# Kernel optimization log

Measured on AMD Instinct MI355X. Metric: run time of the kernel, lower is better.

Reference implementation:

```python
import jax, jax.numpy as jnp
import numpy as np
from jax import lax

B, L, NCH, NQ, NL, FW, NCLS = 256, 3000, 4, 8, 2, 128, 5
BN_EPS = 1e-5


def setup_inputs() -> dict:
    key = jax.random.key(0)
    ks = jax.random.split(key, 24)
    rn = lambda k, shape, s=0.05: jax.random.normal(k, shape, jnp.float32) * s
    inp = {}
    inp['x'] = jax.random.normal(ks[0], (B, NCH, L), jnp.float32)
    inp['conv1_w'] = rn(ks[1], (32, NCH, 7)); inp['conv1_b'] = rn(ks[2], (32,))
    inp['bn1_g'] = 1.0 + rn(ks[3], (32,)); inp['bn1_b'] = rn(ks[3], (32,))
    inp['conv2_w'] = rn(ks[4], (64, 32, 7)); inp['conv2_b'] = rn(ks[5], (64,))
    inp['bn2_g'] = 1.0 + rn(ks[6], (64,)); inp['bn2_b'] = rn(ks[6], (64,))
    inp['conv3_w'] = rn(ks[7], (128, 64, 7)); inp['conv3_b'] = rn(ks[8], (128,))
    inp['bn3_g'] = 1.0 + rn(ks[9], (128,)); inp['bn3_b'] = rn(ks[9], (128,))
    inp['conv4_w'] = rn(ks[10], (128, 128, 7)); inp['conv4_b'] = rn(ks[11], (128,))
    inp['bn4_g'] = 1.0 + rn(ks[12], (128,)); inp['bn4_b'] = rn(ks[12], (128,))
    inp['fc_w'] = rn(ks[13], (FW, 128)); inp['fc_b'] = rn(ks[14], (FW,))
    inp['ang_w'] = rn(ks[15], (NQ, FW)); inp['ang_b'] = rn(ks[16], (NQ,))
    # TorchLayer default init: uniform in [0, 2*pi)
    inp['qw'] = jax.random.uniform(ks[17], (NL, NQ, 3), jnp.float32, 0.0, 2.0 * np.pi)
    inp['h1_w'] = rn(ks[18], (64, NQ)); inp['h1_b'] = rn(ks[19], (64,))
    inp['h2_w'] = rn(ks[20], (NCLS, 64)); inp['h2_b'] = rn(ks[21], (NCLS,))
    return inp


def _conv1d(x, w, b):
    y = lax.conv_general_dilated(x, w, (1,), [(3, 3)], dimension_numbers=('NCH', 'OIH', 'NCH'))
    return y + b[None, :, None]


def _bn(x, g, b):  # eval-mode BN: running_mean=0, running_var=1
    inv = 1.0 / np.sqrt(1.0 + BN_EPS)
    return x * (g * inv)[None, :, None] + b[None, :, None]


def _maxpool4(x):
    return lax.reduce_window(x, -jnp.inf, lax.max, (1, 1, 4), (1, 1, 4), 'VALID')


def _apply_1q(state, U, w, batched):
    # state: (B, 2**NQ); wire 0 = most significant bit (PennyLane convention)
    bs = state.shape[0]
    st = state.reshape(bs, 2 ** w, 2, -1)
    if batched:
        new = jnp.einsum('sab,slbr->slar', U, st)
    else:
        new = jnp.einsum('ab,slbr->slar', U, st)
    return new.reshape(bs, -1)


def _apply_cnot(state, c, t):
    bs = state.shape[0]
    q1, q2 = min(c, t), max(c, t)
    s = state.reshape(bs, 2 ** q1, 2, 2 ** (q2 - q1 - 1), 2, -1)
    ci, ti = (2, 4) if c < t else (4, 2)
    c0 = lax.index_in_dim(s, 0, ci, keepdims=True)
    c1 = jnp.flip(lax.index_in_dim(s, 1, ci, keepdims=True), axis=ti)
    return jnp.concatenate([c0, c1], axis=ci).reshape(bs, -1)


def _rot_matrix(phi, th, om):
    # PennyLane Rot(phi, theta, omega) = RZ(omega) RY(theta) RZ(phi)
    cm, sm = jnp.cos(th / 2), jnp.sin(th / 2)
    m00 = jnp.exp(-0.5j * (phi + om)) * cm
    m01 = -jnp.exp(0.5j * (phi - om)) * sm
    m10 = jnp.exp(-0.5j * (phi - om)) * sm
    m11 = jnp.exp(0.5j * (phi + om)) * cm
    return jnp.stack([jnp.stack([m00, m01]), jnp.stack([m10, m11])]).astype(jnp.complex64)


def _qsim(angles, qw):
    bs = angles.shape[0]
    dim = 2 ** NQ
    state = jnp.zeros((bs, dim), jnp.complex64).at[:, 0].set(1.0)
    # AngleEmbedding: RY(angle_w) on each wire (batched matrices)
    c, s = jnp.cos(angles / 2), jnp.sin(angles / 2)
    for w in range(NQ):
        U = jnp.stack([jnp.stack([c[:, w], -s[:, w]], -1),
                       jnp.stack([s[:, w], c[:, w]], -1)], -2).astype(jnp.complex64)
        state = _apply_1q(state, U, w, batched=True)
    # StronglyEntanglingLayers: Rot on each wire, then CNOT ring with range r
    for l in range(NL):
        for w in range(NQ):
            U = _rot_matrix(qw[l, w, 0], qw[l, w, 1], qw[l, w, 2])
            state = _apply_1q(state, U, w, batched=False)
        r = (l % (NQ - 1)) + 1
        for i in range(NQ):
            state = _apply_cnot(state, i, (i + r) % NQ)
    probs = state.real ** 2 + state.imag ** 2
    z = [probs.reshape(bs, 2 ** w, 2, -1)[:, :, 0].sum((1, 2))
         - probs.reshape(bs, 2 ** w, 2, -1)[:, :, 1].sum((1, 2)) for w in range(NQ)]
    return jnp.stack(z, -1)  # (B, NQ)


def reference(x, conv1_w, conv1_b, bn1_g, bn1_b, conv2_w, conv2_b, bn2_g, bn2_b,
              conv3_w, conv3_b, bn3_g, bn3_b, conv4_w, conv4_b, bn4_g, bn4_b,
              fc_w, fc_b, ang_w, ang_b, qw, h1_w, h1_b, h2_w, h2_b):
    h = jax.nn.relu(_bn(_conv1d(x, conv1_w, conv1_b), bn1_g, bn1_b))
    h = jax.nn.relu(_bn(_conv1d(h, conv2_w, conv2_b), bn2_g, bn2_b))
    h = _maxpool4(h)
    h = jax.nn.relu(_bn(_conv1d(h, conv3_w, conv3_b), bn3_g, bn3_b))
    h = _maxpool4(h)
    h = jax.nn.relu(_bn(_conv1d(h, conv4_w, conv4_b), bn4_g, bn4_b))
    h = h.mean(-1)  # AdaptiveAvgPool1d(1) + Flatten -> (B, 128)
    h = jax.nn.relu(h @ fc_w.T + fc_b)  # Dropout is identity in eval
    raw = h @ ang_w.T + ang_b
    angles = np.pi * jnp.tanh(raw)
    q = _qsim(angles, qw)
    h2 = jax.nn.relu(q @ h1_w.T + h1_b)
    return h2 @ h2_w.T + h2_b
```

## Files before the change

kernel.cpp:

```cpp
#include <hip/hip_runtime.h>
#include <hip/hip_bf16.h>

#define BN_INV 0.9999950000375f
#define PI_F   3.14159265358979f

typedef __attribute__((ext_vector_type(8))) short s16x8;
typedef __attribute__((ext_vector_type(4))) float f32x4;
typedef __attribute__((ext_vector_type(4))) unsigned short u16x4;

__device__ inline unsigned short f2bf(float f) {
  union { float f; unsigned u; } v; v.f = f;
  unsigned r = v.u + 0x7fffu + ((v.u >> 16) & 1u);
  return (unsigned short)(r >> 16);
}

__global__ __launch_bounds__(256) void k_packumat(
    const float* __restrict__ w1, const float* __restrict__ w2,
    const float* __restrict__ w3, const float* __restrict__ w4,
    const float* __restrict__ fcw, const float* __restrict__ qw,
    unsigned short* __restrict__ w1p, unsigned short* __restrict__ w2p,
    unsigned short* __restrict__ w3p, unsigned short* __restrict__ w4p,
    float* __restrict__ fcwt, float* __restrict__ h4,
    float2* __restrict__ Ut)
{
  __shared__ float rotm[16][8];
  const int tid = threadIdx.x;

  if (blockIdx.x < 928) {
    int e = blockIdx.x * 256 + tid;
    if (e < 2048) {
      int co = e >> 6, k = e & 63, kk = k >> 3, ci = k & 7;
      w1p[e] = (ci < 4 && kk < 7) ? f2bf(w1[co * 28 + ci * 7 + kk]) : (unsigned short)0;
    } else if (e < 16384) {
      int t = e - 2048; int co = t / 224, k = t % 224, kk = k >> 5, ci = k & 31;
      w2p[t] = f2bf(w2[co * 224 + ci * 7 + kk]);
    } else if (e < 73728) {
      int t = e - 16384; int co = t / 448, k = t % 448, kk = k >> 6, ci = k & 63;
      w3p[t] = f2bf(w3[co * 448 + ci * 7 + kk]);
    } else if (e < 188416) {
      int t = e - 73728; int co = t / 896, k = t % 896, kk = k >> 7, ci = k & 127;
      w4p[t] = f2bf(w4[co * 896 + ci * 7 + kk]);
    } else if (e < 221184) {
      h4[e - 188416] = 0.f;
    } else if (e < 237568) {
      int t = e - 221184; int k = t >> 7, o = t & 127;
      fcwt[t] = fcw[o * 128 + k];
    }
    return;
  }

  const int bx = blockIdx.x - 928;
  if (tid < 16) {
    int gq = tid;
    float phi = qw[gq * 3], th = qw[gq * 3 + 1], om = qw[gq * 3 + 2];
    float cm = cosf(0.5f * th), sm = sinf(0.5f * th);
    float ap = 0.5f * (phi + om), bm = 0.5f * (phi - om);
    rotm[gq][0] = cm * cosf(ap);  rotm[gq][1] = -cm * sinf(ap);
    rotm[gq][2] = -sm * cosf(bm); rotm[gq][3] = -sm * sinf(bm);
    rotm[gq][4] = sm * cosf(bm);  rotm[gq][5] = -sm * sinf(bm);
    rotm[gq][6] = cm * cosf(ap);  rotm[gq][7] = cm * sinf(ap);
  }
  __syncthreads();

  const int lane = tid & 63, wid = tid >> 6;
  const int ll = lane & 15;
  const int c = (bx * 4 + wid) * 4 + (lane >> 4);

  float2 st[16];
  #pragma unroll
  for (int r = 0; r < 16; ++r) {
    st[r].x = (ll == (c >> 4) && r == (c & 15)) ? 1.f : 0.f;
    st[r].y = 0.f;
  }

#define LOADM(G) \
  float m00x = rotm[G][0], m00y = rotm[G][1], m01x = rotm[G][2], m01y = rotm[G][3], \
        m10x = rotm[G][4], m10y = rotm[G][5], m11x = rotm[G][6], m11y = rotm[G][7];

#define ROT_REG(G, BETA) { LOADM(G) \
  _Pragma("unroll") \
  for (int r = 0; r < 16; ++r) if (!(r & BETA)) { \
    float2 A = st[r], B = st[r + BETA]; \
    st[r].x = m00x*A.x - m00y*A.y + m01x*B.x - m01y*B.y; \
    st[r].y = m00x*A.y + m00y*A.x + m01x*B.y + m01y*B.x; \
    st[r+BETA].x = m10x*A.x - m10y*A.y + m11x*B.x - m11y*B.y; \
    st[r+BETA].y = m10x*A.y + m10y*A.x + m11x*B.y + m11y*B.x; } }

#define ROT_LANE(G, LX) { LOADM(G) \
  _Pragma("unroll") \
  for (int r = 0; r < 16; ++r) { \
    float ox = __shfl_xor(st[r].x, LX); \
    float oy = __shfl_xor(st[r].y, LX); \
    bool hi = (lane & LX) != 0; \
    float a0x = hi ? ox : st[r].x, a0y = hi ? oy : st[r].y; \
    float a1x = hi ? st[r].x : ox, a1y = hi ? st[r].y : oy; \
    float cx = hi ? m10x : m00x, cy = hi ? m10y : m00y; \
    float dx = hi ? m11x : m01x, dy = hi ? m11y : m01y; \
    st[r].x = cx*a0x - cy*a0y + dx*a1x - dy*a1y; \
    st[r].y = cx*a0y + cy*a0x + dx*a1y + dy*a1x; } }

#define CNOT_RR(BC, BT) { \
  _Pragma("unroll") \
  for (int r = 0; r < 16; ++r) if ((r & BC) && !(r & BT)) { \
    float2 t_ = st[r]; st[r] = st[r + BT]; st[r + BT] = t_; } }

#define CNOT_RL(BC, LXT) { \
  _Pragma("unroll") \
  for (int r = 0; r < 16; ++r) if (r & BC) { \
    st[r].x = __shfl_xor(st[r].x, LXT); \
    st[r].y = __shfl_xor(st[r].y, LXT); } }

#define CNOT_LR(LXC, BT) { bool cc = (lane & LXC) != 0; \
  _Pragma("unroll") \
  for (int r = 0; r < 16; ++r) if (!(r & BT)) { \
    float2 A = st[r], B = st[r + BT]; \
    st[r].x = cc ? B.x : A.x;  st[r].y = cc ? B.y : A.y; \
    st[r+BT].x = cc ? A.x : B.x;  st[r+BT].y = cc ? A.y : B.y; } }

#define CNOT_LL(LXC, LXT) { bool cc = (lane & LXC) != 0; \
  _Pragma("unroll") \
  for (int r = 0; r < 16; ++r) { \
    float ox = __shfl_xor(st[r].x, LXT); \
    float oy = __shfl_xor(st[r].y, LXT); \
    if (cc) { st[r].x = ox; st[r].y = oy; } } }

  ROT_LANE(0, 8) ROT_LANE(1, 4) ROT_LANE(2, 2) ROT_LANE(3, 1)
  ROT_REG(4, 8)  ROT_REG(5, 4)  ROT_REG(6, 2)  ROT_REG(7, 1)
  CNOT_LL(8, 4) CNOT_LL(4, 2) CNOT_LL(2, 1) CNOT_LR(1, 8)
  CNOT_RR(8, 4) CNOT_RR(4, 2) CNOT_RR(2, 1) CNOT_RL(1, 8)
  ROT_LANE(8, 8) ROT_LANE(9, 4) ROT_LANE(10, 2) ROT_LANE(11, 1)
  ROT_REG(12, 8) ROT_REG(13, 4) ROT_REG(14, 2)  ROT_REG(15, 1)
  CNOT_LL(8, 2) CNOT_LL(4, 1) CNOT_LR(2, 8) CNOT_LR(1, 4)
  CNOT_RR(8, 2) CNOT_RR(4, 1) CNOT_RL(2, 8) CNOT_RL(1, 4)

#undef LOADM
#undef ROT_REG
#undef ROT_LANE
#undef CNOT_RR
#undef CNOT_RL
#undef CNOT_LR
#undef CNOT_LL

  float2* uc = Ut + c * 256 + ll * 16;
  #pragma unroll
  for (int r = 0; r < 16; r += 2) {
    float4 v = make_float4(st[r].x, st[r].y, st[r + 1].x, st[r + 1].y);
    *(float4*)(uc + r) = v;
  }
}

__global__ __launch_bounds__(512) void k_conv12(
    const float* __restrict__ x, const unsigned short* __restrict__ w1p,
    const unsigned short* __restrict__ w2p,
    const float* __restrict__ c1b, const float* __restrict__ b1g,
    const float* __restrict__ b1b,
    const float* __restrict__ c2b, const float* __restrict__ b2g,
    const float* __restrict__ b2b,
    unsigned short* __restrict__ h2pt)
{
  __shared__ __align__(16) char lds[71296];
  const int XR = 0;
  const int H1 = 8576;
  const int W2 = 41856;
  float* s1 = (float*)(lds + 70528);
  float* s2 = (float*)(lds + 70784);

  const int tid = threadIdx.x, b = blockIdx.y;
  const int l0 = blockIdx.x * 512;

  for (int r = tid; r < 536; r += 512) {
    int gp = l0 - 6 + r;
    s16x8 v;
    for (int i = 0; i < 8; ++i) v[i] = 0;
    if (r < 524 && gp >= 0 && gp < 3000) {
      const float* xr = x + b * 4 * 3000 + gp;
      v[0] = (short)f2bf(xr[0]);
      v[1] = (short)f2bf(xr[3000]);
      v[2] = (short)f2bf(xr[6000]);
      v[3] = (short)f2bf(xr[9000]);
    }
    *(s16x8*)(lds + XR + r * 16) = v;
  }
  for (int e = tid; e < 1792; e += 512) {
    int co = e / 28, cc = e % 28;
    s16x8 v = *(const s16x8*)(w2p + co * 224 + cc * 8);
    *(s16x8*)(lds + W2 + ((co * 448 + cc * 16) ^ ((co & 7) << 4))) = v;
  }
  if (tid < 32) {
    float sc = b1g[tid] * BN_INV;
    s1[tid * 2] = sc;
    s1[tid * 2 + 1] = fmaf(c1b[tid], sc, b1b[tid]);
  }
  if (tid < 64) {
    float sc = b2g[tid] * BN_INV;
    s2[tid * 2] = sc;
    s2[tid * 2 + 1] = fmaf(c2b[tid], sc, b2b[tid]);
  }
  __syncthreads();

  const int w = tid >> 6, lane = tid & 63, lr = lane & 15, g = lane >> 4;

  {
    s16x8 a1[2][2];
    #pragma unroll
    for (int m = 0; m < 2; ++m)
      #pragma unroll
      for (int s = 0; s < 2; ++s)
        a1[m][s] = *(const s16x8*)(w1p + (m * 16 + lr) * 64 + s * 32 + g * 8);

    #pragma unroll
    for (int t = 0; t < 5; ++t) {
      int tile = w + t * 8;
      if (tile >= 33) break;
      int p0 = tile * 16;
      f32x4 acc[2];
      for (int m = 0; m < 2; ++m)
        for (int i = 0; i < 4; ++i) acc[m][i] = 0.f;
      #pragma unroll
      for (int s = 0; s < 2; ++s) {
        s16x8 bf = *(const s16x8*)(lds + XR + (p0 + lr + s * 4 + g) * 16);
        acc[0] = __builtin_amdgcn_mfma_f32_16x16x32_bf16(a1[0][s], bf, acc[0], 0, 0, 0);
        acc[1] = __builtin_amdgcn_mfma_f32_16x16x32_bf16(a1[1][s], bf, acc[1], 0, 0, 0);
      }
      int r2 = p0 + lr;
      if (r2 < 518) {
        #pragma unroll
        for (int m = 0; m < 2; ++m) {
          int co0 = m * 16 + g * 4;
          u16x4 o;
          #pragma unroll
          for (int j = 0; j < 4; ++j)
            o[j] = f2bf(fmaxf(fmaf(acc[m][j], s1[(co0 + j) * 2], s1[(co0 + j) * 2 + 1]), 0.f));
          int byte = ((r2 * 64 + (co0 >> 3) * 16) ^ ((r2 & 7) << 4)) + (co0 & 7) * 2;
          *(u16x4*)(lds + H1 + byte) = o;
        }
      }
    }
  }
  __syncthreads();

  const int wp = w * 64;
  f32x4 acc[4][4];
  for (int m = 0; m < 4; ++m)
    for (int n = 0; n < 4; ++n)
      for (int i = 0; i < 4; ++i) acc[m][n][i] = 0.f;

  #pragma unroll
  for (int s = 0; s < 7; ++s) {
    s16x8 xa[4], wb[4];
    #pragma unroll
    for (int m = 0; m < 4; ++m) {
      int row = wp + m * 16 + lr + s;
      xa[m] = *(const s16x8*)(lds + H1 + ((row * 64 + g * 16) ^ ((row & 7) << 4)));
    }
    #pragma unroll
    for (int n = 0; n < 4; ++n) {
      int co = n * 16 + lr;
      wb[n] = *(const s16x8*)(lds + W2 + ((co * 448 + s * 64 + g * 16) ^ ((co & 7) << 4)));
    }
    #pragma unroll
    for (int m = 0; m < 4; ++m)
      #pragma unroll
      for (int n = 0; n < 4; ++n)
        acc[m][n] = __builtin_amdgcn_mfma_f32_16x16x32_bf16(xa[m], wb[n], acc[m][n], 0, 0, 0);
  }

  float sc[4], sh[4];
  #pragma unroll
  for (int n = 0; n < 4; ++n) {
    sc[n] = s2[(n * 16 + lr) * 2];
    sh[n] = s2[(n * 16 + lr) * 2 + 1];
  }
  #pragma unroll
  for (int m = 0; m < 4; ++m) {
    int pp = (l0 + wp + m * 16 + g * 4) >> 2;
    if (pp < 750) {
      unsigned short* orow = h2pt + (b * 750 + pp) * 64 + lr;
      #pragma unroll
      for (int n = 0; n < 4; ++n) {
        float v = fmaxf(fmaxf(acc[m][n][0], acc[m][n][1]),
                        fmaxf(acc[m][n][2], acc[m][n][3]));
        orow[n * 16] = f2bf(fmaxf(fmaf(v, sc[n], sh[n]), 0.f));
      }
    }
  }
}

__global__ __launch_bounds__(256) void k_conv3(
    const unsigned short* __restrict__ h2pt, const unsigned short* __restrict__ w3p,
    const float* __restrict__ cb, const float* __restrict__ bng,
    const float* __restrict__ bnb, unsigned short* __restrict__ h3pt)
{
  __shared__ __align__(16) char lds[75776];
  float* scs = (float*)(lds + 74752);
  const int tid = threadIdx.x, b = blockIdx.y;
  const int l0 = blockIdx.x * 128;

  for (int e = tid; e < 1072; e += 256) {
    int r = e >> 3, c = e & 7;
    int gr = l0 + r - 3;
    s16x8 v;
    if (gr >= 0 && gr < 750) v = *(const s16x8*)(h2pt + (b * 750 + gr) * 64 + c * 8);
    else for (int i = 0; i < 8; ++i) v[i] = 0;
    *(s16x8*)(lds + ((r * 128 + c * 16) ^ ((r & 7) << 4))) = v;
  }
  for (int e = tid; e < 3584; e += 256) {
    int co = e / 28, c = e % 28;
    s16x8 v = *(const s16x8*)(w3p + co * 448 + c * 8);
    *(s16x8*)(lds + 17408 + ((co * 448 + c * 16) ^ ((co & 7) << 4))) = v;
  }
  if (tid < 128) {
    float sc = bng[tid] * BN_INV;
    scs[tid * 2] = sc;
    scs[tid * 2 + 1] = fmaf(cb[tid], sc, bnb[tid]);
  }

  const int lane = tid & 63, wid = tid >> 6;
  const int wr = wid >> 1, wc = wid & 1;
  const int lr = lane & 15, g = lane >> 4;

  f32x4 acc[4][4];
  for (int m = 0; m < 4; ++m)
    for (int n = 0; n < 4; ++n)
      for (int i = 0; i < 4; ++i) acc[m][n][i] = 0.f;

  s16x8 pw[14];
  #pragma unroll
  for (int i = 0; i < 14; ++i) {
    int e = tid + i * 256;
    int co = e / 28, c = e % 28;
    pw[i] = *(const s16x8*)(w3p + co * 448 + 224 + c * 8);
  }
  __syncthreads();

  for (int chunk = 0; chunk < 2; ++chunk) {
    #pragma unroll
    for (int sl = 0; sl < 7; ++sl) {
      int k0 = chunk * 224 + sl * 32;
      int kk = k0 >> 6, cib = k0 & 63;
      s16x8 xa[4], wb[4];
      #pragma unroll
      for (int m = 0; m < 4; ++m) {
        int row = wr * 64 + m * 16 + lr + kk;
        xa[m] = *(const s16x8*)(lds + ((row * 128 + cib * 2 + g * 16) ^ ((row & 7) << 4)));
      }
      #pragma unroll
      for (int n = 0; n < 4; ++n) {
        int co = wc * 64 + n * 16 + lr;
        wb[n] = *(const s16x8*)(lds + 17408 + ((co * 448 + sl * 64 + g * 16) ^ ((co & 7) << 4)));
      }
      #pragma unroll
      for (int m = 0; m < 4; ++m)
        #pragma unroll
        for (int n = 0; n < 4; ++n)
          acc[m][n] = __builtin_amdgcn_mfma_f32_16x16x32_bf16(xa[m], wb[n], acc[m][n], 0, 0, 0);
    }
    if (chunk == 0) {
      __syncthreads();
      #pragma unroll
      for (int i = 0; i < 14; ++i) {
        int e = tid + i * 256;
        int co = e / 28, c = e % 28;
        *(s16x8*)(lds + 17408 + ((co * 448 + c * 16) ^ ((co & 7) << 4))) = pw[i];
      }
      __syncthreads();
    }
  }

  float sc[4], sh[4];
  #pragma unroll
  for (int n = 0; n < 4; ++n) {
    int co = wc * 64 + n * 16 + lr;
    sc[n] = scs[co * 2];
    sh[n] = scs[co * 2 + 1];
  }
  #pragma unroll
  for (int m = 0; m < 4; ++m) {
    int pp = (l0 + wr * 64 + m * 16 + g * 4) >> 2;
    if (pp < 187) {
      unsigned short* orow = h3pt + (b * 187 + pp) * 128;
      #pragma unroll
      for (int n = 0; n < 4; ++n) {
        int co = wc * 64 + n * 16 + lr;
        float v = fmaxf(fmaxf(acc[m][n][0], acc[m][n][1]),
                        fmaxf(acc[m][n][2], acc[m][n][3]));
        orow[co] = f2bf(fmaxf(fmaf(v, sc[n], sh[n]), 0.f));
      }
    }
  }
}

__global__ __launch_bounds__(256) void k_conv4(
    const unsigned short* __restrict__ h3pt, const unsigned short* __restrict__ w4p,
    const float* __restrict__ cb, const float* __restrict__ bng,
    const float* __restrict__ bnb, float* __restrict__ h4)
{
  __shared__ __align__(16) char lds[79872];
  float* scs = (float*)(lds + 79360);
  const int tid = threadIdx.x, b = blockIdx.y, ch = blockIdx.x;
  const int cg0 = ch * 64;

  #pragma unroll
  for (int i = 0; i < 13; ++i) {
    int e = tid + i * 256;
    if (e < 3168) {
      int r = e >> 4, c = e & 15, gr = r - 3;
      s16x8 v;
      if (gr >= 0 && gr < 187) v = *(const s16x8*)(h3pt + (b * 187 + gr) * 128 + c * 8);
      else for (int q = 0; q < 8; ++q) v[q] = 0;
      *(s16x8*)(lds + ((r * 256 + c * 16) ^ ((r & 7) << 4))) = v;
    }
  }
  for (int e = tid; e < 1792; e += 256) {
    int co = e / 28, c = e % 28;
    s16x8 v = *(const s16x8*)(w4p + (cg0 + co) * 896 + c * 8);
    *(s16x8*)(lds + 50688 + ((co * 448 + c * 16) ^ ((co & 7) << 4))) = v;
  }
  if (tid < 64) {
    int co = cg0 + tid;
    float sc = bng[co] * BN_INV;
    scs[tid * 2] = sc;
    scs[tid * 2 + 1] = fmaf(cb[co], sc, bnb[co]);
  }
  __syncthreads();

  const int w = tid >> 6, l = tid & 63, lr = l & 15, g = l >> 4;
  const int wp = w * 48;

  f32x4 acc[3][4];
  for (int m = 0; m < 3; ++m)
    for (int n = 0; n < 4; ++n)
      for (int i = 0; i < 4; ++i) acc[m][n][i] = 0.f;

  for (int chunk = 0; chunk < 4; ++chunk) {
    s16x8 wr[7];
    if (chunk < 3) {
      #pragma unroll
      for (int i = 0; i < 7; ++i) {
        int e = tid + i * 256;
        int co = e / 28, c = e % 28;
        wr[i] = *(const s16x8*)(w4p + (cg0 + co) * 896 + (chunk + 1) * 224 + c * 8);
      }
    }
    #pragma unroll
    for (int sl = 0; sl < 7; ++sl) {
      int k0 = chunk * 224 + sl * 32;
      int kk = k0 >> 7, cib = k0 & 127;
      s16x8 xa[3], wb[4];
      #pragma unroll
      for (int m = 0; m < 3; ++m) {
        int row = wp + m * 16 + lr + kk;
        xa[m] = *(const s16x8*)(lds + ((row * 256 + cib * 2 + g * 16) ^ ((row & 7) << 4)));
      }
      #pragma unroll
      for (int n = 0; n < 4; ++n) {
        int co = n * 16 + lr;
        wb[n] = *(const s16x8*)(lds + 50688 + ((co * 448 + sl * 64 + g * 16) ^ ((co & 7) << 4)));
      }
      #pragma unroll
      for (int m = 0; m < 3; ++m)
        #pragma unroll
        for (int n = 0; n < 4; ++n)
          acc[m][n] = __builtin_amdgcn_mfma_f32_16x16x32_bf16(xa[m], wb[n], acc[m][n], 0, 0, 0);
    }
    __syncthreads();
    if (chunk < 3) {
      #pragma unroll
      for (int i = 0; i < 7; ++i) {
        int e = tid + i * 256;
        int co = e / 28, c = e % 28;
        *(s16x8*)(lds + 50688 + ((co * 448 + c * 16) ^ ((co & 7) << 4))) = wr[i];
      }
    }
    __syncthreads();
  }

  float sc[4], sh[4];
  #pragma unroll
  for (int n = 0; n < 4; ++n) {
    sc[n] = scs[(n * 16 + lr) * 2];
    sh[n] = scs[(n * 16 + lr) * 2 + 1];
  }
  float psum[4] = {0.f, 0.f, 0.f, 0.f};
  #pragma unroll
  for (int m = 0; m < 3; ++m) {
    #pragma unroll
    for (int j = 0; j < 4; ++j) {
      int pos = wp + m * 16 + g * 4 + j;
      if (pos < 187) {
        #pragma unroll
        for (int n = 0; n < 4; ++n)
          psum[n] += fmaxf(fmaf(acc[m][n][j], sc[n], sh[n]), 0.f);
      }
    }
  }
  #pragma unroll
  for (int n = 0; n < 4; ++n) {
    float v = psum[n];
    v += __shfl_xor(v, 16);
    v += __shfl_xor(v, 32);
    if (l < 16)
      atomicAdd(&h4[b * 128 + cg0 + n * 16 + lr], v);
  }
}

__global__ __launch_bounds__(256) void k_head2(
    const float* __restrict__ h4, const float* __restrict__ fc_wt,
    const float* __restrict__ fc_b, const float* __restrict__ ang_w,
    const float* __restrict__ ang_b, const float* __restrict__ h1_w,
    const float* __restrict__ h1_b, const float* __restrict__ h2_w,
    const float* __restrict__ h2_b, const float2* __restrict__ Ut,
    float* __restrict__ out)
{
  __shared__ float h4v[512];
  __shared__ float fvec[512];
  __shared__ float rcs[64];
  __shared__ float4 e4[256];
  __shared__ float4 parr[256];
  __shared__ float zsum[32];
  __shared__ float hh[256];

  const int tid = threadIdx.x;
  const int b0 = blockIdx.x * 4;

  #pragma unroll
  for (int q = 0; q < 2; ++q) {
    int task = tid + q * 256;
    h4v[task] = h4[(b0 + (task >> 7)) * 128 + (task & 127)] * (1.0f / 187.0f);
  }
  __syncthreads();

  #pragma unroll
  for (int q = 0; q < 2; ++q) {
    int task = tid + q * 256;
    int bb = task >> 7, o = task & 127;
    float a = fc_b[o];
    const float* hv = h4v + bb * 128;
    #pragma unroll 8
    for (int k = 0; k < 128; ++k) a = fmaf(hv[k], fc_wt[k * 128 + o], a);
    fvec[task] = fmaxf(a, 0.f);
  }
  __syncthreads();

  if (tid < 32) {
    int bb = tid >> 3, o = tid & 7;
    float a = ang_b[o];
    const float* fv = fvec + bb * 128;
    const float* wr = ang_w + o * 128;
    for (int k = 0; k < 128; ++k) a = fmaf(fv[k], wr[k], a);
    float ang = PI_F * tanhf(a);
    rcs[bb * 16 + o * 2]     = cosf(0.5f * ang);
    rcs[bb * 16 + o * 2 + 1] = sinf(0.5f * ang);
  }
  __syncthreads();

  {
    float4 ev;
    #pragma unroll
    for (int bb = 0; bb < 4; ++bb) {
      float prod = 1.f;
      #pragma unroll
      for (int w = 0; w < 8; ++w) {
        float cc = rcs[bb * 16 + w * 2];
        float ss = rcs[bb * 16 + w * 2 + 1];
        prod *= ((tid >> (7 - w)) & 1) ? ss : cc;
      }
      ev[bb] = prod;
    }
    e4[tid] = ev;
  }
  __syncthreads();

  {
    float ax0 = 0.f, ax1 = 0.f, ax2 = 0.f, ax3 = 0.f;
    float ay0 = 0.f, ay1 = 0.f, ay2 = 0.f, ay3 = 0.f;
    #pragma unroll 4
    for (int cc = 0; cc < 256; ++cc) {
      float2 u = Ut[cc * 256 + tid];
      float4 ev = e4[cc];
      ax0 = fmaf(u.x, ev[0], ax0); ay0 = fmaf(u.y, ev[0], ay0);
      ax1 = fmaf(u.x, ev[1], ax1); ay1 = fmaf(u.y, ev[1], ay1);
      ax2 = fmaf(u.x, ev[2], ax2); ay2 = fmaf(u.y, ev[2], ay2);
      ax3 = fmaf(u.x, ev[3], ax3); ay3 = fmaf(u.y, ev[3], ay3);
    }
    parr[tid] = make_float4(ax0 * ax0 + ay0 * ay0, ax1 * ax1 + ay1 * ay1,
                            ax2 * ax2 + ay2 * ay2, ax3 * ax3 + ay3 * ay3);
  }
  __syncthreads();

  {
    int task = tid >> 3, part = tid & 7;
    int bb = task >> 3, wq = task & 7;
    int bit = 7 - wq;
    float s = 0.f;
    #pragma unroll 8
    for (int i = 0; i < 32; ++i) {
      int row = i * 8 + part;
      const float* pr = (const float*)&parr[row];
      float p = pr[bb];
      s = ((row >> bit) & 1) ? (s - p) : (s + p);
    }
    s += __shfl_xor(s, 1);
    s += __shfl_xor(s, 2);
    s += __shfl_xor(s, 4);
    if (part == 0) zsum[task] = s;
  }
  __syncthreads();

  {
    int bb = tid >> 6, o = tid & 63;
    float a = h1_b[o];
    #pragma unroll
    for (int k = 0; k < 8; ++k) a = fmaf(zsum[bb * 8 + k], h1_w[o * 8 + k], a);
    hh[tid] = fmaxf(a, 0.f);
  }
  __syncthreads();

  if (tid < 20) {
    int bb = tid / 5, o = tid % 5;
    float a = h2_b[o];
    for (int j = 0; j < 64; ++j) a = fmaf(hh[bb * 64 + j], h2_w[o * 64 + j], a);
    out[(b0 + bb) * 5 + o] = a;
  }
}

extern "C" void kernel_launch(void* const* d_in, const int* in_sizes, int n_in,
                              void* d_out, int out_size, void* d_ws, size_t ws_size,
                              hipStream_t stream) {
  (void)in_sizes; (void)n_in; (void)out_size; (void)ws_size;
  const float* x    = (const float*)d_in[0];
  const float* c1w  = (const float*)d_in[1];
  const float* c1b  = (const float*)d_in[2];
  const float* b1g  = (const float*)d_in[3];
  const float* b1b  = (const float*)d_in[4];
  const float* c2w  = (const float*)d_in[5];
  const float* c2b  = (const float*)d_in[6];
  const float* b2g  = (const float*)d_in[7];
  const float* b2b  = (const float*)d_in[8];
  const float* c3w  = (const float*)d_in[9];
  const float* c3b  = (const float*)d_in[10];
  const float* b3g  = (const float*)d_in[11];
  const float* b3b  = (const float*)d_in[12];
  const float* c4w  = (const float*)d_in[13];
  const float* c4b  = (const float*)d_in[14];
  const float* b4g  = (const float*)d_in[15];
  const float* b4b  = (const float*)d_in[16];
  const float* fcw  = (const float*)d_in[17];
  const float* fcb  = (const float*)d_in[18];
  const float* angw = (const float*)d_in[19];
  const float* angb = (const float*)d_in[20];
  const float* qw   = (const float*)d_in[21];
  const float* h1w  = (const float*)d_in[22];
  const float* h1b  = (const float*)d_in[23];
  const float* h2w  = (const float*)d_in[24];
  const float* h2b  = (const float*)d_in[25];

  char* wsb = (char*)d_ws;
  unsigned short* w1p  = (unsigned short*)(wsb + 0);
  unsigned short* w2p  = (unsigned short*)(wsb + 4096);
  unsigned short* w3p  = (unsigned short*)(wsb + 32768);
  unsigned short* w4p  = (unsigned short*)(wsb + 147456);
  float*          h4   = (float*)(wsb + 393216);
  unsigned short* h2pt = (unsigned short*)(wsb + 52428800);
  unsigned short* h3pt = (unsigned short*)(wsb + 79691776);
  float2*         Ut   = (float2*)(wsb + 100663296);
  float*          fcwt = (float*)(wsb + 101187584);

  k_packumat<<<dim3(944), 256, 0, stream>>>(c1w, c2w, c3w, c4w, fcw, qw,
                                            w1p, w2p, w3p, w4p, fcwt, h4, Ut);
  k_conv12<<<dim3(6, 256), 512, 0, stream>>>(x, w1p, w2p, c1b, b1g, b1b,
                                             c2b, b2g, b2b, h2pt);
  k_conv3<<<dim3(6, 256), 256, 0, stream>>>(h2pt, w3p, c3b, b3g, b3b, h3pt);
  k_conv4<<<dim3(2, 256), 256, 0, stream>>>(h3pt, w4p, c4b, b4g, b4b, h4);
  k_head2<<<dim3(64), 256, 0, stream>>>(h4, fcwt, fcb, angw, angb,
                                        h1w, h1b, h2w, h2b, Ut, (float*)d_out);
}
```

Measured before the change: 229.8 us.

## Stream conv weights from global into registers instead of staging in LDS

In conv2, conv3 and conv4, the weight operand for each MFMA k-slice is now loaded straight from global memory into registers, with a one-slice-ahead prefetch, instead of being copied into shared memory and read back. This removes the LDS weight buffers, the staging loops and the intra-loop barriers in conv3 and conv4, and shrinks LDS use, which can allow more blocks per CU. The cost is more global/L2 traffic: every wave re-fetches the weight fragments, and load latency is only hidden by a single-stage prefetch.

```diff
diff --git a/kernel.cpp b/kernel.cpp
--- a/kernel.cpp
+++ b/kernel.cpp
@@ -158,12 +158,11 @@
     const float* __restrict__ b2b,
     unsigned short* __restrict__ h2pt)
 {
-  __shared__ __align__(16) char lds[71296];
+  __shared__ __align__(16) char lds[42624];
   const int XR = 0;
   const int H1 = 8576;
-  const int W2 = 41856;
-  float* s1 = (float*)(lds + 70528);
-  float* s2 = (float*)(lds + 70784);
+  float* s1 = (float*)(lds + 41856);
+  float* s2 = (float*)(lds + 42112);
 
   const int tid = threadIdx.x, b = blockIdx.y;
   const int l0 = blockIdx.x * 512;
@@ -180,11 +179,6 @@
       v[3] = (short)f2bf(xr[9000]);
     }
     *(s16x8*)(lds + XR + r * 16) = v;
-  }
-  for (int e = tid; e < 1792; e += 512) {
-    int co = e / 28, cc = e % 28;
-    s16x8 v = *(const s16x8*)(w2p + co * 224 + cc * 8);
-    *(s16x8*)(lds + W2 + ((co * 448 + cc * 16) ^ ((co & 7) << 4))) = v;
   }
   if (tid < 32) {
     float sc = b1g[tid] * BN_INV;
@@ -245,24 +239,31 @@
     for (int n = 0; n < 4; ++n)
       for (int i = 0; i < 4; ++i) acc[m][n][i] = 0.f;
 
+  s16x8 wcur[4], wnxt[4];
+  #pragma unroll
+  for (int n = 0; n < 4; ++n)
+    wcur[n] = *(const s16x8*)(w2p + (n * 16 + lr) * 224 + g * 8);
+
   #pragma unroll
   for (int s = 0; s < 7; ++s) {
-    s16x8 xa[4], wb[4];
+    if (s < 6) {
+      #pragma unroll
+      for (int n = 0; n < 4; ++n)
+        wnxt[n] = *(const s16x8*)(w2p + (n * 16 + lr) * 224 + (s + 1) * 32 + g * 8);
+    }
+    s16x8 xa[4];
     #pragma unroll
     for (int m = 0; m < 4; ++m) {
       int row = wp + m * 16 + lr + s;
       xa[m] = *(const s16x8*)(lds + H1 + ((row * 64 + g * 16) ^ ((row & 7) << 4)));
     }
     #pragma unroll
-    for (int n = 0; n < 4; ++n) {
-      int co = n * 16 + lr;
-      wb[n] = *(const s16x8*)(lds + W2 + ((co * 448 + s * 64 + g * 16) ^ ((co & 7) << 4)));
-    }
-    #pragma unroll
     for (int m = 0; m < 4; ++m)
       #pragma unroll
       for (int n = 0; n < 4; ++n)
-        acc[m][n] = __builtin_amdgcn_mfma_f32_16x16x32_bf16(xa[m], wb[n], acc[m][n], 0, 0, 0);
+        acc[m][n] = __builtin_amdgcn_mfma_f32_16x16x32_bf16(xa[m], wcur[n], acc[m][n], 0, 0, 0);
+    #pragma unroll
+    for (int n = 0; n < 4; ++n) wcur[n] = wnxt[n];
   }
 
   float sc[4], sh[4];
@@ -291,8 +292,8 @@
     const float* __restrict__ cb, const float* __restrict__ bng,
     const float* __restrict__ bnb, unsigned short* __restrict__ h3pt)
 {
-  __shared__ __align__(16) char lds[75776];
-  float* scs = (float*)(lds + 74752);
+  __shared__ __align__(16) char lds[18432];
+  float* scs = (float*)(lds + 17408);
   const int tid = threadIdx.x, b = blockIdx.y;
   const int l0 = blockIdx.x * 128;
 
@@ -304,11 +305,6 @@
     else for (int i = 0; i < 8; ++i) v[i] = 0;
     *(s16x8*)(lds + ((r * 128 + c * 16) ^ ((r & 7) << 4))) = v;
   }
-  for (int e = tid; e < 3584; e += 256) {
-    int co = e / 28, c = e % 28;
-    s16x8 v = *(const s16x8*)(w3p + co * 448 + c * 8);
-    *(s16x8*)(lds + 17408 + ((co * 448 + c * 16) ^ ((co & 7) << 4))) = v;
-  }
   if (tid < 128) {
     float sc = bng[tid] * BN_INV;
     scs[tid * 2] = sc;
@@ -324,47 +320,33 @@
     for (int n = 0; n < 4; ++n)
       for (int i = 0; i < 4; ++i) acc[m][n][i] = 0.f;
 
-  s16x8 pw[14];
-  #pragma unroll
-  for (int i = 0; i < 14; ++i) {
-    int e = tid + i * 256;
-    int co = e / 28, c = e % 28;
-    pw[i] = *(const s16x8*)(w3p + co * 448 + 224 + c * 8);
-  }
-  __syncthreads();
-
-  for (int chunk = 0; chunk < 2; ++chunk) {
-    #pragma unroll
-    for (int sl = 0; sl < 7; ++sl) {
-      int k0 = chunk * 224 + sl * 32;
-      int kk = k0 >> 6, cib = k0 & 63;
-      s16x8 xa[4], wb[4];
-      #pragma unroll
-      for (int m = 0; m < 4; ++m) {
-        int row = wr * 64 + m * 16 + lr + kk;
-        xa[m] = *(const s16x8*)(lds + ((row * 128 + cib * 2 + g * 16) ^ ((row & 7) << 4)));
-      }
-      #pragma unroll
-      for (int n = 0; n < 4; ++n) {
-        int co = wc * 64 + n * 16 + lr;
-        wb[n] = *(const s16x8*)(lds + 17408 + ((co * 448 + sl * 64 + g * 16) ^ ((co & 7) << 4)));
-      }
-      #pragma unroll
-      for (int m = 0; m < 4; ++m)
-        #pragma unroll
-        for (int n = 0; n < 4; ++n)
-          acc[m][n] = __builtin_amdgcn_mfma_f32_16x16x32_bf16(xa[m], wb[n], acc[m][n], 0, 0, 0);
-    }
-    if (chunk == 0) {
-      __syncthreads();
-      #pragma unroll
-      for (int i = 0; i < 14; ++i) {
-        int e = tid + i * 256;
-        int co = e / 28, c = e % 28;
-        *(s16x8*)(lds + 17408 + ((co * 448 + c * 16) ^ ((co & 7) << 4))) = pw[i];
-      }
-      __syncthreads();
-    }
+  s16x8 wcur[4], wnxt[4];
+  #pragma unroll
+  for (int n = 0; n < 4; ++n)
+    wcur[n] = *(const s16x8*)(w3p + (wc * 64 + n * 16 + lr) * 448 + g * 8);
+  __syncthreads();
+
+  #pragma unroll
+  for (int sl = 0; sl < 14; ++sl) {
+    if (sl < 13) {
+      #pragma unroll
+      for (int n = 0; n < 4; ++n)
+        wnxt[n] = *(const s16x8*)(w3p + (wc * 64 + n * 16 + lr) * 448 + (sl + 1) * 32 + g * 8);
+    }
+    int kk = sl >> 1, cib = (sl & 1) * 32;
+    s16x8 xa[4];
+    #pragma unroll
+    for (int m = 0; m < 4; ++m) {
+      int row = wr * 64 + m * 16 + lr + kk;
+      xa[m] = *(const s16x8*)(lds + ((row * 128 + cib * 2 + g * 16) ^ ((row & 7) << 4)));
+    }
+    #pragma unroll
+    for (int m = 0; m < 4; ++m)
+      #pragma unroll
+      for (int n = 0; n < 4; ++n)
+        acc[m][n] = __builtin_amdgcn_mfma_f32_16x16x32_bf16(xa[m], wcur[n], acc[m][n], 0, 0, 0);
+    #pragma unroll
+    for (int n = 0; n < 4; ++n) wcur[n] = wnxt[n];
   }
 
   float sc[4], sh[4];
@@ -395,8 +377,8 @@
     const float* __restrict__ cb, const float* __restrict__ bng,
     const float* __restrict__ bnb, float* __restrict__ h4)
 {
-  __shared__ __align__(16) char lds[79872];
-  float* scs = (float*)(lds + 79360);
+  __shared__ __align__(16) char lds[51200];
+  float* scs = (float*)(lds + 50688);
   const int tid = threadIdx.x, b = blockIdx.y, ch = blockIdx.x;
   const int cg0 = ch * 64;
 
@@ -411,18 +393,12 @@
       *(s16x8*)(lds + ((r * 256 + c * 16) ^ ((r & 7) << 4))) = v;
     }
   }
-  for (int e = tid; e < 1792; e += 256) {
-    int co = e / 28, c = e % 28;
-    s16x8 v = *(const s16x8*)(w4p + (cg0 + co) * 896 + c * 8);
-    *(s16x8*)(lds + 50688 + ((co * 448 + c * 16) ^ ((co & 7) << 4))) = v;
-  }
   if (tid < 64) {
     int co = cg0 + tid;
     float sc = bng[co] * BN_INV;
     scs[tid * 2] = sc;
     scs[tid * 2 + 1] = fmaf(cb[co], sc, bnb[co]);
   }
-  __syncthreads();
 
   const int w = tid >> 6, l = tid & 63, lr = l & 15, g = l >> 4;
   const int wp = w * 48;
@@ -432,47 +408,33 @@
     for (int n = 0; n < 4; ++n)
       for (int i = 0; i < 4; ++i) acc[m][n][i] = 0.f;
 
-  for (int chunk = 0; chunk < 4; ++chunk) {
-    s16x8 wr[7];
-    if (chunk < 3) {
-      #pragma unroll
-      for (int i = 0; i < 7; ++i) {
-        int e = tid + i * 256;
-        int co = e / 28, c = e % 28;
-        wr[i] = *(const s16x8*)(w4p + (cg0 + co) * 896 + (chunk + 1) * 224 + c * 8);
-      }
-    }
-    #pragma unroll
-    for (int sl = 0; sl < 7; ++sl) {
-      int k0 = chunk * 224 + sl * 32;
-      int kk = k0 >> 7, cib = k0 & 127;
-      s16x8 xa[3], wb[4];
-      #pragma unroll
-      for (int m = 0; m < 3; ++m) {
-        int row = wp + m * 16 + lr + kk;
-        xa[m] = *(const s16x8*)(lds + ((row * 256 + cib * 2 + g * 16) ^ ((row & 7) << 4)));
-      }
-      #pragma unroll
-      for (int n = 0; n < 4; ++n) {
-        int co = n * 16 + lr;
-        wb[n] = *(const s16x8*)(lds + 50688 + ((co * 448 + sl * 64 + g * 16) ^ ((co & 7) << 4)));
-      }
-      #pragma unroll
-      for (int m = 0; m < 3; ++m)
-        #pragma unroll
-        for (int n = 0; n < 4; ++n)
-          acc[m][n] = __builtin_amdgcn_mfma_f32_16x16x32_bf16(xa[m], wb[n], acc[m][n], 0, 0, 0);
-    }
-    __syncthreads();
-    if (chunk < 3) {
-      #pragma unroll
-      for (int i = 0; i < 7; ++i) {
-        int e = tid + i * 256;
-        int co = e / 28, c = e % 28;
-        *(s16x8*)(lds + 50688 + ((co * 448 + c * 16) ^ ((co & 7) << 4))) = wr[i];
-      }
-    }
-    __syncthreads();
+  s16x8 wcur[4], wnxt[4];
+  #pragma unroll
+  for (int n = 0; n < 4; ++n)
+    wcur[n] = *(const s16x8*)(w4p + (cg0 + n * 16 + lr) * 896 + g * 8);
+  __syncthreads();
+
+  #pragma unroll 4
+  for (int sl = 0; sl < 28; ++sl) {
+    if (sl < 27) {
+      #pragma unroll
+      for (int n = 0; n < 4; ++n)
+        wnxt[n] = *(const s16x8*)(w4p + (cg0 + n * 16 + lr) * 896 + (sl + 1) * 32 + g * 8);
+    }
+    int kk = sl >> 2, cib = (sl & 3) * 32;
+    s16x8 xa[3];
+    #pragma unroll
+    for (int m = 0; m < 3; ++m) {
+      int row = wp + m * 16 + lr + kk;
+      xa[m] = *(const s16x8*)(lds + ((row * 256 + cib * 2 + g * 16) ^ ((row & 7) << 4)));
+    }
+    #pragma unroll
+    for (int m = 0; m < 3; ++m)
+      #pragma unroll
+      for (int n = 0; n < 4; ++n)
+        acc[m][n] = __builtin_amdgcn_mfma_f32_16x16x32_bf16(xa[m], wcur[n], acc[m][n], 0, 0, 0);
+    #pragma unroll
+    for (int n = 0; n < 4; ++n) wcur[n] = wnxt[n];
   }
 
   float sc[4], sh[4];
```

After: 278.5 us. +21.2%, slower.
